# Kernel optimization log

Measured on AMD Instinct MI355X. Metric: run time of the kernel, lower is better.

The kernel has to match this reference:

```python
import jax, jax.numpy as jnp
import numpy as np

D_MODEL = 2048
N_EXPERTS = 8
LOSS_SCALE = 3e-06


def setup_inputs() -> dict:
    key = jax.random.key(0)
    k_x, k_wr, k_br, k_w, k_b = jax.random.split(key, 5)
    s = 1.0 / np.sqrt(D_MODEL)
    x = jax.random.normal(k_x, (4, 2048, D_MODEL), dtype=jnp.float32)
    # router: nn.Linear(D, E) -> weight (E, D), bias (E,)
    Wr = jax.random.uniform(k_wr, (N_EXPERTS, D_MODEL), dtype=jnp.float32, minval=-s, maxval=s)
    br = jax.random.uniform(k_br, (N_EXPERTS,), dtype=jnp.float32, minval=-s, maxval=s)
    # experts: E stacked nn.Linear(D, D) -> weight (E, D_out, D_in), bias (E, D)
    W = jax.random.uniform(k_w, (N_EXPERTS, D_MODEL, D_MODEL), dtype=jnp.float32, minval=-s, maxval=s)
    b = jax.random.uniform(k_b, (N_EXPERTS, D_MODEL), dtype=jnp.float32, minval=-s, maxval=s)
    return {"x": x, "Wr": Wr, "br": br, "W": W, "b": b}


def reference(x, Wr, br, W, b):
    B, S, D = x.shape
    E = Wr.shape[0]
    xt = x.reshape(B * S, D)          # (T, D)
    T = xt.shape[0]

    logits = xt @ Wr.T + br           # (T, E)
    probs = jax.nn.softmax(logits, axis=-1)
    idx = jnp.argmax(probs, axis=-1)  # top-1 expert per token
    topp = jnp.max(probs, axis=-1)    # gating weight
    onehot = jax.nn.one_hot(idx, E, dtype=xt.dtype)  # (T, E)

    # auxiliary load-balancing loss (matches torch compute_loss exactly)
    fractions = onehot.mean(axis=0)                              # (E,)
    probability = (onehot * topp[:, None]).sum(axis=0) / (T * T)  # (E,)
    loss = jnp.sum(fractions * probability) * LOSS_SCALE * E

    # all-expert outputs then top-1 select (dense grouped GEMM form)
    y_all = jnp.einsum('td,efd->tef', xt, W) + b[None, :, :]     # (T, E, D)
    y = jnp.einsum('tef,te->tf', y_all, onehot) * topp[:, None]  # (T, D)
    return y.reshape(B, S, D), loss
```

## Files before the change

kernel.cpp:

```cpp
#include <hip/hip_runtime.h>

typedef unsigned short u16;
typedef unsigned int u32;
typedef __attribute__((ext_vector_type(8))) __bf16 bf16x8;
typedef __attribute__((ext_vector_type(4))) float f32x4;

#define T_TOK 8192
#define DMODEL 2048
#define N_EXP 8

__device__ __forceinline__ u32 f2bf_bits(float f) {
    u32 u = __builtin_bit_cast(u32, f);
    return (u + 0x7fffu + ((u >> 16) & 1u)) >> 16;
}
__device__ __forceinline__ u32 pack2(float a, float b) {
    return f2bf_bits(a) | (f2bf_bits(b) << 16);
}

__device__ __forceinline__ void load_lds16(const u16* g, u16* l) {
    void* gnc = (void*)g;
    __builtin_amdgcn_global_load_lds(
        (__attribute__((address_space(1))) void*)gnc,
        (__attribute__((address_space(3))) void*)l,
        16, 0, 0);
}

__global__ void zero_kernel(u32* p) {
    p[threadIdx.x] = 0u;
}

__global__ void __launch_bounds__(256) convert_w_kernel(const float* __restrict__ W,
                                                        u16* __restrict__ Wb) {
    size_t i = ((size_t)blockIdx.x * 256 + threadIdx.x) * 8;
    float4 a = *(const float4*)(W + i);
    float4 b = *(const float4*)(W + i + 4);
    uint4 o;
    o.x = pack2(a.x, a.y);
    o.y = pack2(a.z, a.w);
    o.z = pack2(b.x, b.y);
    o.w = pack2(b.z, b.w);
    *(uint4*)(Wb + i) = o;
}

__global__ void __launch_bounds__(256) router_kernel(const float* __restrict__ x,
                                                     const float* __restrict__ Wr,
                                                     const float* __restrict__ br,
                                                     u16* __restrict__ xb,
                                                     int* __restrict__ perm,
                                                     float* __restrict__ topp,
                                                     int* __restrict__ counts,
                                                     float* __restrict__ sumt) {
    __shared__ int sEid[4];
    __shared__ float sTp[4];

    int tid = threadIdx.x;
    int lane = tid & 63;
    int w = tid >> 6;
    int t = blockIdx.x * 4 + w;

    const float4* xp = (const float4*)(x + ((size_t)t << 11));
    u16* xbp = xb + ((size_t)t << 11);

    float acc[8];
#pragma unroll
    for (int e = 0; e < 8; e++) acc[e] = 0.0f;

#pragma unroll
    for (int i = 0; i < 8; i++) {
        int vidx = i * 64 + lane;
        float4 xv = xp[vidx];
        uint2 pk;
        pk.x = pack2(xv.x, xv.y);
        pk.y = pack2(xv.z, xv.w);
        *(uint2*)(xbp + (size_t)vidx * 4) = pk;
#pragma unroll
        for (int e = 0; e < 8; e++) {
            float4 wv = *(const float4*)(Wr + e * DMODEL + vidx * 4);
            acc[e] = fmaf(xv.x, wv.x, fmaf(xv.y, wv.y,
                      fmaf(xv.z, wv.z, fmaf(xv.w, wv.w, acc[e]))));
        }
    }
#pragma unroll
    for (int off = 32; off; off >>= 1)
#pragma unroll
        for (int e = 0; e < 8; e++)
            acc[e] += __shfl_xor(acc[e], off, 64);

    if (lane == 0) {
        float lg[8];
#pragma unroll
        for (int e = 0; e < 8; e++) lg[e] = acc[e] + br[e];
        float m = lg[0];
        int am = 0;
#pragma unroll
        for (int e = 1; e < 8; e++)
            if (lg[e] > m) { m = lg[e]; am = e; }
        float s = 0.0f;
#pragma unroll
        for (int e = 0; e < 8; e++) s += __expf(lg[e] - m);
        float tp = 1.0f / s;
        sEid[w] = am;
        sTp[w] = tp;
        topp[t] = tp;
    }
    __syncthreads();
    if (tid < 4) {
        int e = sEid[tid];
        float tp = sTp[tid];
        int pos = atomicAdd(&counts[e * 16], 1);
        perm[(e << 13) + pos] = blockIdx.x * 4 + tid;
        atomicAdd(&sumt[e * 16], tp);
    }
}

__global__ void __launch_bounds__(256) moe_gemm_kernel(const u16* __restrict__ xb,
                                                       const u16* __restrict__ Wb,
                                                       const float* __restrict__ bias,
                                                       const int* __restrict__ perm,
                                                       const int* __restrict__ counts,
                                                       const float* __restrict__ topp,
                                                       float* __restrict__ out) {
    __shared__ __align__(16) u16 ldsA[8192];
    __shared__ __align__(16) u16 ldsB[8192];

    int bid = blockIdx.x;
    int tr = bid >> 7;
    int e  = (bid >> 4) & 7;
    int tc = bid & 15;
    int cnt = counts[e * 16];
    int row0 = tr << 7;
    if (row0 >= cnt) return;
    int n0 = tc << 7;

    int tid = threadIdx.x;
    int lane = tid & 63;
    int w = tid >> 6;

    const int* permE = perm + (e << 13);
    const u16* WbE = Wb + ((size_t)e << 22);
    const u16* gA[4]; u16* lA[4];
    const u16* gB[4]; u16* lB[4];
#pragma unroll
    for (int j = 0; j < 4; j++) {
        int s = tid + j * 256;
        int r = s >> 3;
        int cg = (s & 7) ^ (r & 7);
        int ta = permE[min(row0 + r, cnt - 1)];
        gA[j] = xb + ((size_t)ta << 11) + (cg << 3);
        gB[j] = WbE + ((size_t)(n0 + r) << 11) + (cg << 3);
        lA[j] = ldsA + s * 8;
        lB[j] = ldsB + s * 8;
    }

    int mbase = (w & 1) << 6;
    int nbase = (w >> 1) << 6;
    int mrow = lane & 15;
    int kq = lane >> 4;
    int s7 = mrow & 7;

    f32x4 acc[4][4];
#pragma unroll
    for (int mi = 0; mi < 4; mi++)
#pragma unroll
        for (int ni = 0; ni < 4; ni++)
            acc[mi][ni] = (f32x4){0.0f, 0.0f, 0.0f, 0.0f};

    for (int kt = 0; kt < DMODEL / 64; kt++) {
        int ko = kt << 6;
#pragma unroll
        for (int j = 0; j < 4; j++) load_lds16(gA[j] + ko, lA[j]);
#pragma unroll
        for (int j = 0; j < 4; j++) load_lds16(gB[j] + ko, lB[j]);
        __syncthreads();

#pragma unroll
        for (int ks = 0; ks < 2; ks++) {
            int kcs = (ks * 4 + kq) ^ s7;
            int aO = ((mbase + mrow) * 8 + kcs) * 8;
            int bO = ((nbase + mrow) * 8 + kcs) * 8;
            bf16x8 af[4], bf[4];
#pragma unroll
            for (int i = 0; i < 4; i++) {
                af[i] = *(const bf16x8*)(ldsA + aO + i * 1024);
                bf[i] = *(const bf16x8*)(ldsB + bO + i * 1024);
            }
#pragma unroll
            for (int mi = 0; mi < 4; mi++)
#pragma unroll
                for (int ni = 0; ni < 4; ni++)
                    acc[mi][ni] = __builtin_amdgcn_mfma_f32_16x16x32_bf16(
                        af[mi], bf[ni], acc[mi][ni], 0, 0, 0);
        }
        __syncthreads();
    }

    const float* bE = bias + (e << 11);
    float bv[4];
#pragma unroll
    for (int ni = 0; ni < 4; ni++)
        bv[ni] = bE[n0 + nbase + ni * 16 + (lane & 15)];

    int rb = row0 + mbase + ((lane >> 4) << 2);
#pragma unroll
    for (int mi = 0; mi < 4; mi++) {
        int t_[4]; float tp_[4]; int v_[4];
#pragma unroll
        for (int r = 0; r < 4; r++) {
            int gr = rb + mi * 16 + r;
            v_[r] = gr < cnt;
            int grc = v_[r] ? gr : (cnt - 1);
            t_[r] = permE[grc];
            tp_[r] = topp[t_[r]];
        }
#pragma unroll
        for (int ni = 0; ni < 4; ni++) {
            int col = n0 + nbase + ni * 16 + (lane & 15);
            f32x4 v = acc[mi][ni];
#pragma unroll
            for (int r = 0; r < 4; r++) {
                if (v_[r])
                    out[((size_t)t_[r] << 11) + col] = (v[r] + bv[ni]) * tp_[r];
            }
        }
    }
}

__global__ void loss_kernel(const int* __restrict__ counts,
                            const float* __restrict__ sumt,
                            float* __restrict__ lossOut) {
    if (threadIdx.x == 0) {
        float acc = 0.0f;
        for (int e = 0; e < 8; e++) {
            float frac = (float)counts[e * 16] / 8192.0f;
            float prob = sumt[e * 16] / (8192.0f * 8192.0f);
            acc = fmaf(frac, prob, acc);
        }
        lossOut[0] = acc * 3e-6f * 8.0f;
    }
}

extern "C" void kernel_launch(void* const* d_in, const int* in_sizes, int n_in,
                              void* d_out, int out_size, void* d_ws, size_t ws_size,
                              hipStream_t stream) {
    const float* x  = (const float*)d_in[0];
    const float* Wr = (const float*)d_in[1];
    const float* br = (const float*)d_in[2];
    const float* W  = (const float*)d_in[3];
    const float* b  = (const float*)d_in[4];
    float* out = (float*)d_out;

    char* ws = (char*)d_ws;
    u16* Wb     = (u16*)ws;
    u16* xb     = (u16*)(ws + 67108864);
    int* perm   = (int*)(ws + 100663296);
    float* topp = (float*)(ws + 100925440);
    int* counts = (int*)(ws + 100958208);
    float* sumt = (float*)(ws + 100958720);

    zero_kernel<<<1, 256, 0, stream>>>((u32*)counts);
    convert_w_kernel<<<(8 * 2048 * 2048) / (256 * 8), 256, 0, stream>>>(W, Wb);
    router_kernel<<<T_TOK / 4, 256, 0, stream>>>(x, Wr, br, xb, perm, topp, counts, sumt);
    moe_gemm_kernel<<<N_EXP * 64 * 16, 256, 0, stream>>>(xb, Wb, b, perm, counts, topp, out);
    loss_kernel<<<1, 64, 0, stream>>>(counts, sumt, out + (size_t)T_TOK * DMODEL);
}
```

Before: 412.2 us.

## Double-buffer MoE GEMM LDS loads, reorder block mapping, batch router tokens

```diff
diff --git a/kernel.cpp b/kernel.cpp
--- a/kernel.cpp
+++ b/kernel.cpp
@@ -50,65 +50,76 @@
                                                      float* __restrict__ topp,
                                                      int* __restrict__ counts,
                                                      float* __restrict__ sumt) {
-    __shared__ int sEid[4];
-    __shared__ float sTp[4];
+    __shared__ int sEid[16];
+    __shared__ float sTp[16];
 
     int tid = threadIdx.x;
     int lane = tid & 63;
     int w = tid >> 6;
-    int t = blockIdx.x * 4 + w;
-
-    const float4* xp = (const float4*)(x + ((size_t)t << 11));
-    u16* xbp = xb + ((size_t)t << 11);
-
-    float acc[8];
-#pragma unroll
-    for (int e = 0; e < 8; e++) acc[e] = 0.0f;
+    int t0 = blockIdx.x * 16 + w * 4;
+
+    float acc[4][8];
+#pragma unroll
+    for (int tk = 0; tk < 4; tk++)
+#pragma unroll
+        for (int e = 0; e < 8; e++) acc[tk][e] = 0.0f;
 
 #pragma unroll
     for (int i = 0; i < 8; i++) {
         int vidx = i * 64 + lane;
-        float4 xv = xp[vidx];
-        uint2 pk;
-        pk.x = pack2(xv.x, xv.y);
-        pk.y = pack2(xv.z, xv.w);
-        *(uint2*)(xbp + (size_t)vidx * 4) = pk;
-#pragma unroll
-        for (int e = 0; e < 8; e++) {
-            float4 wv = *(const float4*)(Wr + e * DMODEL + vidx * 4);
-            acc[e] = fmaf(xv.x, wv.x, fmaf(xv.y, wv.y,
-                      fmaf(xv.z, wv.z, fmaf(xv.w, wv.w, acc[e]))));
+        float4 wv[8];
+#pragma unroll
+        for (int e = 0; e < 8; e++)
+            wv[e] = *(const float4*)(Wr + e * DMODEL + vidx * 4);
+#pragma unroll
+        for (int tk = 0; tk < 4; tk++) {
+            int t = t0 + tk;
+            float4 xv = ((const float4*)(x + ((size_t)t << 11)))[vidx];
+            uint2 pk;
+            pk.x = pack2(xv.x, xv.y);
+            pk.y = pack2(xv.z, xv.w);
+            *(uint2*)(xb + ((size_t)t << 11) + (size_t)vidx * 4) = pk;
+#pragma unroll
+            for (int e = 0; e < 8; e++) {
+                acc[tk][e] = fmaf(xv.x, wv[e].x, fmaf(xv.y, wv[e].y,
+                              fmaf(xv.z, wv[e].z, fmaf(xv.w, wv[e].w, acc[tk][e]))));
+            }
         }
     }
 #pragma unroll
     for (int off = 32; off; off >>= 1)
 #pragma unroll
-        for (int e = 0; e < 8; e++)
-            acc[e] += __shfl_xor(acc[e], off, 64);
+        for (int tk = 0; tk < 4; tk++)
+#pragma unroll
+            for (int e = 0; e < 8; e++)
+                acc[tk][e] += __shfl_xor(acc[tk][e], off, 64);
 
     if (lane == 0) {
-        float lg[8];
-#pragma unroll
-        for (int e = 0; e < 8; e++) lg[e] = acc[e] + br[e];
-        float m = lg[0];
-        int am = 0;
-#pragma unroll
-        for (int e = 1; e < 8; e++)
-            if (lg[e] > m) { m = lg[e]; am = e; }
-        float s = 0.0f;
-#pragma unroll
-        for (int e = 0; e < 8; e++) s += __expf(lg[e] - m);
-        float tp = 1.0f / s;
-        sEid[w] = am;
-        sTp[w] = tp;
-        topp[t] = tp;
+#pragma unroll
+        for (int tk = 0; tk < 4; tk++) {
+            float lg[8];
+#pragma unroll
+            for (int e = 0; e < 8; e++) lg[e] = acc[tk][e] + br[e];
+            float m = lg[0];
+            int am = 0;
+#pragma unroll
+            for (int e = 1; e < 8; e++)
+                if (lg[e] > m) { m = lg[e]; am = e; }
+            float s = 0.0f;
+#pragma unroll
+            for (int e = 0; e < 8; e++) s += __expf(lg[e] - m);
+            float tp = 1.0f / s;
+            sEid[w * 4 + tk] = am;
+            sTp[w * 4 + tk] = tp;
+            topp[t0 + tk] = tp;
+        }
     }
     __syncthreads();
-    if (tid < 4) {
+    if (tid < 16) {
         int e = sEid[tid];
         float tp = sTp[tid];
         int pos = atomicAdd(&counts[e * 16], 1);
-        perm[(e << 13) + pos] = blockIdx.x * 4 + tid;
+        perm[(e << 13) + pos] = blockIdx.x * 16 + tid;
         atomicAdd(&sumt[e * 16], tp);
     }
 }
@@ -120,13 +131,12 @@
                                                        const int* __restrict__ counts,
                                                        const float* __restrict__ topp,
                                                        float* __restrict__ out) {
-    __shared__ __align__(16) u16 ldsA[8192];
-    __shared__ __align__(16) u16 ldsB[8192];
+    __shared__ __align__(16) u16 lds[32768];
 
     int bid = blockIdx.x;
+    int e  = bid & 7;
+    int tc = (bid >> 3) & 15;
     int tr = bid >> 7;
-    int e  = (bid >> 4) & 7;
-    int tc = bid & 15;
     int cnt = counts[e * 16];
     int row0 = tr << 7;
     if (row0 >= cnt) return;
@@ -138,8 +148,9 @@
 
     const int* permE = perm + (e << 13);
     const u16* WbE = Wb + ((size_t)e << 22);
-    const u16* gA[4]; u16* lA[4];
-    const u16* gB[4]; u16* lB[4];
+    const u16* gA[4];
+    const u16* gB[4];
+    int sOff[4];
 #pragma unroll
     for (int j = 0; j < 4; j++) {
         int s = tid + j * 256;
@@ -148,8 +159,7 @@
         int ta = permE[min(row0 + r, cnt - 1)];
         gA[j] = xb + ((size_t)ta << 11) + (cg << 3);
         gB[j] = WbE + ((size_t)(n0 + r) << 11) + (cg << 3);
-        lA[j] = ldsA + s * 8;
-        lB[j] = ldsB + s * 8;
+        sOff[j] = s * 8;
     }
 
     int mbase = (w & 1) << 6;
@@ -165,14 +175,29 @@
         for (int ni = 0; ni < 4; ni++)
             acc[mi][ni] = (f32x4){0.0f, 0.0f, 0.0f, 0.0f};
 
-    for (int kt = 0; kt < DMODEL / 64; kt++) {
-        int ko = kt << 6;
-#pragma unroll
-        for (int j = 0; j < 4; j++) load_lds16(gA[j] + ko, lA[j]);
-#pragma unroll
-        for (int j = 0; j < 4; j++) load_lds16(gB[j] + ko, lB[j]);
-        __syncthreads();
-
+#pragma unroll
+    for (int j = 0; j < 4; j++) load_lds16(gA[j], lds + sOff[j]);
+#pragma unroll
+    for (int j = 0; j < 4; j++) load_lds16(gB[j], lds + 16384 + sOff[j]);
+
+    for (int kt = 0; kt < 32; kt++) {
+        int p = kt & 1;
+        if (kt < 31) {
+            int ko = (kt + 1) << 6;
+            u16* la = lds + (p ^ 1) * 8192;
+            u16* lb = lds + 16384 + (p ^ 1) * 8192;
+#pragma unroll
+            for (int j = 0; j < 4; j++) load_lds16(gA[j] + ko, la + sOff[j]);
+#pragma unroll
+            for (int j = 0; j < 4; j++) load_lds16(gB[j] + ko, lb + sOff[j]);
+            asm volatile("s_waitcnt vmcnt(8)" ::: "memory");
+        } else {
+            asm volatile("s_waitcnt vmcnt(0)" ::: "memory");
+        }
+        asm volatile("s_barrier" ::: "memory");
+
+        const u16* bufA = lds + p * 8192;
+        const u16* bufB = lds + 16384 + p * 8192;
 #pragma unroll
         for (int ks = 0; ks < 2; ks++) {
             int kcs = (ks * 4 + kq) ^ s7;
@@ -181,8 +206,8 @@
             bf16x8 af[4], bf[4];
 #pragma unroll
             for (int i = 0; i < 4; i++) {
-                af[i] = *(const bf16x8*)(ldsA + aO + i * 1024);
-                bf[i] = *(const bf16x8*)(ldsB + bO + i * 1024);
+                af[i] = *(const bf16x8*)(bufA + aO + i * 1024);
+                bf[i] = *(const bf16x8*)(bufB + bO + i * 1024);
             }
 #pragma unroll
             for (int mi = 0; mi < 4; mi++)
@@ -191,7 +216,7 @@
                     acc[mi][ni] = __builtin_amdgcn_mfma_f32_16x16x32_bf16(
                         af[mi], bf[ni], acc[mi][ni], 0, 0, 0);
         }
-        __syncthreads();
+        asm volatile("s_barrier" ::: "memory");
     }
 
     const float* bE = bias + (e << 11);
@@ -259,7 +284,7 @@
 
     zero_kernel<<<1, 256, 0, stream>>>((u32*)counts);
     convert_w_kernel<<<(8 * 2048 * 2048) / (256 * 8), 256, 0, stream>>>(W, Wb);
-    router_kernel<<<T_TOK / 4, 256, 0, stream>>>(x, Wr, br, xb, perm, topp, counts, sumt);
+    router_kernel<<<T_TOK / 16, 256, 0, stream>>>(x, Wr, br, xb, perm, topp, counts, sumt);
     moe_gemm_kernel<<<N_EXP * 64 * 16, 256, 0, stream>>>(xb, Wb, b, perm, counts, topp, out);
     loss_kernel<<<1, 64, 0, stream>>>(counts, sumt, out + (size_t)T_TOK * DMODEL);
 }
```

After: 411.5 us. About the same (-0.2%).
